# Kernel tuning notes

Measured on AMD Instinct MI355X. Metric: run time of the kernel, lower is better.

Reference implementation:

```python
import jax, jax.numpy as jnp
import numpy as np
from jax import lax

L = 5; HID = 100; B = 4; H = 256; W = 256; MU = 0.02; SLOPE = 0.01

def conv2d(x, w, pad=1, groups=1):
    return lax.conv_general_dilated(x, w, (1, 1), ((pad, pad), (pad, pad)),
                                    dimension_numbers=('NCHW', 'OIHW', 'NCHW'),
                                    feature_group_count=groups)

def leaky(x):
    return jnp.where(x >= 0, x, SLOPE * x)

def res_block(x, w1, w2, w3):
    # dropout omitted (eval-mode reference)
    h = leaky(conv2d(x, w1))
    h = leaky(conv2d(h, w2))
    return conv2d(h, w3)

def gauss1d(size=51, sigma=10.0):
    x = jnp.arange(size, dtype=jnp.float32) - (size - 1) / 2.0
    g = jnp.exp(-0.5 * (x / sigma) ** 2)
    return g / g.sum()

def gaussian_blur(x):
    # kornia GaussianBlur2d((51,51),(10,10), border 'constant') == zero-pad separable blur
    C = x.shape[1]
    g = gauss1d()
    kh = jnp.tile(g.reshape(1, 1, 1, 51), (C, 1, 1, 1))
    kv = jnp.tile(g.reshape(1, 1, 51, 1), (C, 1, 1, 1))
    x = lax.conv_general_dilated(x, kh, (1, 1), ((0, 0), (25, 25)),
                                 dimension_numbers=('NCHW', 'OIHW', 'NCHW'), feature_group_count=C)
    x = lax.conv_general_dilated(x, kv, (1, 1), ((25, 25), (0, 0)),
                                 dimension_numbers=('NCHW', 'OIHW', 'NCHW'), feature_group_count=C)
    return x

def spatial_gradient(x):
    # kornia SpatialGradient('sobel', normalized): kernels /8, replicate padding -> [B,C,2,H,W]
    Bk, C, Hk, Wk = x.shape
    kx = jnp.array([[-1., 0., 1.], [-2., 0., 2.], [-1., 0., 1.]], dtype=x.dtype) / 8.0
    k = jnp.stack([kx, kx.T])[:, None]          # [2,1,3,3]
    k = jnp.tile(k, (C, 1, 1, 1))               # [2C,1,3,3]
    xp = jnp.pad(x, ((0, 0), (0, 0), (1, 1), (1, 1)), mode='edge')
    out = conv2d(xp, k, pad=0, groups=C)        # [B,2C,H,W]
    return out.reshape(Bk, C, 2, Hk, Wk)

def deform_image(img, grid):
    # img [B,C,H,W]; grid [B,2,H,W] pixel coords (x,y); bilinear grid_sample, zeros outside
    Bk, C, Hk, Wk = img.shape
    x, y = grid[:, 0], grid[:, 1]
    x0 = jnp.floor(x); y0 = jnp.floor(y)
    wx1 = x - x0; wy1 = y - y0
    flat = img.reshape(Bk, C, Hk * Wk)
    def tap(xi, yi, wgt):
        valid = (xi >= 0) & (xi <= Wk - 1) & (yi >= 0) & (yi <= Hk - 1)
        xc = jnp.clip(xi, 0, Wk - 1).astype(jnp.int32)
        yc = jnp.clip(yi, 0, Hk - 1).astype(jnp.int32)
        idx = (yc * Wk + xc).reshape(Bk, 1, Hk * Wk)
        v = jnp.take_along_axis(flat, idx, axis=2).reshape(Bk, C, Hk, Wk)
        return v * (wgt * valid.astype(img.dtype))[:, None]
    return (tap(x0, y0, (1 - wx1) * (1 - wy1)) + tap(x0 + 1, y0, wx1 * (1 - wy1))
            + tap(x0, y0 + 1, (1 - wx1) * wy1) + tap(x0 + 1, y0 + 1, wx1 * wy1))

def forward(source, source_seg, z0, zw1, zw2, zw3, vw1, vw2, vw3):
    Bk, _, Hk, Wk = source.shape
    l = zw1.shape[0]
    yy, xx = jnp.meshgrid(jnp.arange(Hk, dtype=source.dtype), jnp.arange(Wk, dtype=source.dtype), indexing='ij')
    deformation = jnp.broadcast_to(jnp.stack([xx, yy])[None], (Bk, 2, Hk, Wk))  # pixel-coord id grid
    images = [source]
    residuals = [jnp.broadcast_to(z0, (Bk,) + z0.shape[1:])]
    residuals_deformed = [residuals[0]]
    fields = []
    grads = [spatial_gradient(source)]
    for i in range(l):
        zin = jnp.concatenate([residuals[i], images[i], images[0]], axis=1)  # 3 channels
        f = res_block(zin, zw1[i], zw2[i], zw3[i]) / l
        residuals.append(residuals[i] + f)
        residuals_deformed = [deform_image(z, deformation) for z in residuals_deformed]
        residuals_deformed.append(residuals[-1])
        vin = jnp.concatenate([deformation, images[-1]], axis=1)  # 3 channels
        fields.append(gaussian_blur(res_block(vin, vw1[i], vw2[i], vw3[i])))
        deformation = deformation - fields[i] / l
        mask = deform_image(source_seg, deformation)
        acc = residuals_deformed[1]
        for z in residuals_deformed[2:]:
            acc = acc + z
        new_img = deform_image(images[0], deformation) + acc * (MU ** 2 / l) * mask
        images.append(new_img)
        grads.append(spatial_gradient(new_img))
    return jnp.stack(images), jnp.stack(fields), jnp.stack(residuals), jnp.stack(grads)

def setup_inputs() -> dict:
    key = jax.random.key(0)
    ks = jax.random.split(key, 9)
    def rn(k, shape, s):
        return s * jax.random.normal(k, shape, dtype=jnp.float32)
    return {
        'source': rn(ks[0], (B, 1, H, W), 1.0),
        'source_seg': jax.random.uniform(ks[1], (B, 1, H, W), dtype=jnp.float32),
        'z0': rn(ks[2], (1, 1, H, W), 0.05),
        'zw1': rn(ks[3], (L, HID, 3, 3, 3), 0.2),
        'zw2': rn(ks[4], (L, HID, HID, 3, 3), 0.033),
        'zw3': rn(ks[5], (L, 1, HID, 3, 3), 0.033),
        'vw1': rn(ks[6], (L, HID, 3, 3, 3), 0.02),
        'vw2': rn(ks[7], (L, HID, HID, 3, 3), 0.033),
        'vw3': rn(ks[8], (L, 2, HID, 3, 3), 0.033),
    }

def reference(source, source_seg, z0, zw1, zw2, zw3, vw1, vw2, vw3):
    return forward(source, source_seg, z0, zw1, zw2, zw3, vw1, vw2, vw3)
```

## Files before the change

### kernel.cpp

```cpp
#include <hip/hip_runtime.h>
#include <math.h>

#define HW 65536
#define BB 4
#define NL 5

typedef short s8v __attribute__((ext_vector_type(8)));
typedef float f4v __attribute__((ext_vector_type(4)));
typedef unsigned short u16;

#define AS1 __attribute__((address_space(1)))
#define AS3 __attribute__((address_space(3)))

__device__ __forceinline__ float leaky_f(float x){ return x >= 0.f ? x : 0.01f * x; }

__device__ __forceinline__ u16 f2bf(float x){
    union { float f; unsigned u; } v; v.f = x;
    unsigned r = v.u + 0x7FFF + ((v.u >> 16) & 1);
    return (u16)(r >> 16);
}
__device__ __forceinline__ float bf2f(u16 h){
    union { unsigned u; float f; } v; v.u = ((unsigned)h) << 16;
    return v.f;
}

__global__ void k_init(const float* __restrict__ src, const float* __restrict__ z0,
                       float* __restrict__ images0, float* __restrict__ resid0,
                       float* __restrict__ def){
    int p = blockIdx.x * 256 + threadIdx.x;
    int b = p >> 16, q = p & 65535;
    images0[p] = src[p];
    resid0[p]  = z0[q];
    int x = q & 255, y = q >> 8;
    def[(size_t)(b * 2 + 0) * HW + q] = (float)x;
    def[(size_t)(b * 2 + 1) * HW + q] = (float)y;
}

__global__ void k_grad(const float* __restrict__ img, float* __restrict__ gout){
    int p = blockIdx.x * 256 + threadIdx.x;
    int b = p >> 16, q = p & 65535;
    int x = q & 255, y = q >> 8;
    const float* ib = img + (size_t)b * HW;
    int xm = max(x - 1, 0), xp = min(x + 1, 255);
    int ym = max(y - 1, 0), yp = min(y + 1, 255);
    float a00 = ib[ym * 256 + xm], a01 = ib[ym * 256 + x], a02 = ib[ym * 256 + xp];
    float a10 = ib[y  * 256 + xm],                         a12 = ib[y  * 256 + xp];
    float a20 = ib[yp * 256 + xm], a21 = ib[yp * 256 + x], a22 = ib[yp * 256 + xp];
    float gx = (a02 - a00 + 2.f * (a12 - a10) + a22 - a20) * 0.125f;
    float gy = (a20 - a00 + 2.f * (a21 - a01) + a22 - a02) * 0.125f;
    gout[(size_t)(b * 2 + 0) * HW + q] = gx;
    gout[(size_t)(b * 2 + 1) * HW + q] = gy;
}

__global__ void k_packw(const float* __restrict__ zw2, const float* __restrict__ vw2,
                        u16* __restrict__ wp){
    int idx = blockIdx.x * 256 + threadIdx.x;
    int lane9 = idx & 511, chunk = idx >> 9;
    int nt = chunk % 7; int t = chunk / 7;
    int ks = t % 4; t >>= 2;
    int off = t % 9; t /= 9;
    int layer = t % 5, path = t / 5;
    int lane = lane9 >> 3, j = lane9 & 7;
    int ic = ks * 32 + (lane >> 4) * 8 + j;
    int oc = nt * 16 + (lane & 15);
    const float* w = path ? vw2 : zw2;
    float v = 0.f;
    if (ic < 100 && oc < 100)
        v = w[(((size_t)layer * 100 + oc) * 100 + ic) * 9 + off];
    wp[idx] = f2bf(v);
}

__global__ void k_packw3(const float* __restrict__ zw3, const float* __restrict__ vw3,
                         u16* __restrict__ wq){
    int idx = blockIdx.x * 256 + threadIdx.x;
    if (idx >= 184320) return;
    int lane9 = idx & 511, chunk = idx >> 9;
    int ks = chunk & 3; int t = chunk >> 2;
    int off = t % 9; int slot = t / 9;
    int lane = lane9 >> 3, j = lane9 & 7;
    int ic = ks * 32 + (lane >> 4) * 8 + j;
    int oc = lane & 15;
    float v = 0.f;
    if (ic < 100){
        if (slot < 5){ if (oc == 0) v = zw3[((size_t)slot * 100 + ic) * 9 + off]; }
        else { int layer = slot - 5;
               if (oc < 2) v = vw3[(((size_t)layer * 2 + oc) * 100 + ic) * 9 + off]; }
    }
    wq[idx] = f2bf(v);
}

__global__ __launch_bounds__(256)
void k_conv1(const float* __restrict__ p0, int s0, const float* __restrict__ p1, int s1,
             const float* __restrict__ p2, int s2, const float* __restrict__ w1,
             u16* __restrict__ h1, int b0){
    __shared__ float t3[300];
    __shared__ float wl[2700];
    const int tid = threadIdx.x;
    const int tX = blockIdx.x, tY = blockIdx.y, bz = blockIdx.z;
    const int b = b0 + bz;
    const int y0 = tY * 8 - 1, x0 = tX * 8 - 1;
    for (int idx = tid; idx < 300; idx += 256){
        int ch = idx / 100, p = idx - ch * 100;
        int r = p / 10, c = p - r * 10;
        int gy = y0 + r, gx = x0 + c;
        const float* pp = (ch == 0) ? p0 + (size_t)b * s0
                        : (ch == 1) ? p1 + (size_t)b * s1 : p2 + (size_t)b * s2;
        t3[idx] = ((unsigned)gy < 256u && (unsigned)gx < 256u) ? pp[gy * 256 + gx] : 0.f;
    }
    for (int idx = tid; idx < 2700; idx += 256) wl[idx] = w1[idx];
    __syncthreads();

    const int px = tid & 63, g = tid >> 6;
    const int row = px >> 3, colx = px & 7;
    float iv[27];
    #pragma unroll
    for (int c3 = 0; c3 < 3; c3++)
        #pragma unroll
        for (int dr = 0; dr < 3; dr++)
            #pragma unroll
            for (int dc = 0; dc < 3; dc++)
                iv[c3 * 9 + dr * 3 + dc] = t3[c3 * 100 + (row + dr) * 10 + colx + dc];

    const int gy = tY * 8 + row, gx = tX * 8 + colx;
    u16* dst = h1 + (((size_t)bz * HW + (size_t)(gy * 256 + gx)) << 7) + g * 32;
    #pragma unroll
    for (int s = 0; s < 4; s++){
        int ov[4];
        #pragma unroll
        for (int hp = 0; hp < 4; hp++){
            u16 lo = 0, hi = 0;
            #pragma unroll
            for (int e = 0; e < 2; e++){
                int oc = g * 32 + s * 8 + hp * 2 + e;
                u16 hv = 0;
                if (oc < 100){
                    const float* wk = &wl[oc * 27];
                    float a = 0.f;
                    #pragma unroll
                    for (int q = 0; q < 27; q++) a = fmaf(wk[q], iv[q], a);
                    hv = f2bf(leaky_f(a));
                }
                if (e) hi = hv; else lo = hv;
            }
            ov[hp] = (int)lo | ((int)hi << 16);
        }
        *(int4*)(dst + s * 8) = make_int4(ov[0], ov[1], ov[2], ov[3]);
    }
}

__device__ __forceinline__ void dma_setup(const u16* __restrict__ h, size_t hbase,
                                          int y0, int x0, int tid,
                                          const u16** gp, int* gstep){
    const u16* zpad = h + (hbase << 7) + 112;
    #pragma unroll
    for (int s = 0; s < 6; s++){
        int idx = tid + s * 256;
        const u16* g = zpad; int st = 0;
        if (idx < 1360){
            int px = idx >> 2, part = idx & 3;
            int hr = px / 34, hc = px - hr * 34;
            int gy = y0 + hr, gx = x0 + hc;
            if ((unsigned)gy < 256u && (unsigned)gx < 256u){
                g = h + ((hbase + (size_t)(gy * 256 + gx)) << 7) + (part ^ ((px >> 1) & 3)) * 8;
                st = 32;
            }
        }
        gp[s] = g; gstep[s] = st;
    }
}

__device__ __forceinline__ void dma_slab(const u16** gp, const int* gstep,
                                         short* Lnxt, int wv){
    #pragma unroll
    for (int s = 0; s < 6; s++){
        __builtin_amdgcn_global_load_lds(
            (const AS1 unsigned int*)(unsigned long long)(const void*)gp[s],
            (AS3 unsigned int*)(unsigned long long)(void*)(&Lnxt[(s * 256 + wv * 64) * 8]),
            16, 0, 0);
        gp[s] += gstep[s];
    }
}

__global__ __launch_bounds__(256, 2)
void k_conv2(const u16* __restrict__ h1, const u16* __restrict__ wp, u16* __restrict__ h2){
    __shared__ __align__(16) short lds[2][12288];
    const int tid = threadIdx.x;
    const int lane = tid & 63, wv = tid >> 6;
    const int quad = lane >> 4, m = lane & 15;
    const int tX = blockIdx.x, tY = blockIdx.y, bz = blockIdx.z;
    const int y0 = tY * 8 - 1, x0 = tX * 32 - 1;
    const size_t hbase = (size_t)bz << 16;

    f4v acc[4][7];
    #pragma unroll
    for (int t = 0; t < 4; t++)
        #pragma unroll
        for (int n = 0; n < 7; n++){
            acc[t][n][0] = 0.f; acc[t][n][1] = 0.f; acc[t][n][2] = 0.f; acc[t][n][3] = 0.f;
        }

    const u16* gp[6]; int gstep[6];
    dma_setup(h1, hbase, y0, x0, tid, gp, gstep);
    dma_slab(gp, gstep, lds[0], wv);

    for (int ks = 0; ks < 4; ks++){
        __syncthreads();
        const short* L = lds[ks & 1];
        short* Lnxt = lds[(ks + 1) & 1];
        const bool pre = (ks < 3);
        #pragma unroll
        for (int off = 0; off < 9; off++){
            if (off == 4 && pre) dma_slab(gp, gstep, Lnxt, wv);
            const int dr = off / 3, dc = off - dr * 3;
            s8v bf[4];
            #pragma unroll
            for (int t = 0; t < 4; t++){
                int hpx = (2 * wv + (t >> 1) + dr) * 34 + (t & 1) * 16 + dc + m;
                bf[t] = *(const s8v*)&L[hpx * 32 + ((quad ^ ((hpx >> 1) & 3)) << 3)];
            }
            const u16* wb = wp + (size_t)((off * 4 + ks) * 7) * 512 + lane * 8;
            #pragma unroll
            for (int nt = 0; nt < 7; nt++){
                s8v af = *(const s8v*)(wb + nt * 512);
                #pragma unroll
                for (int t = 0; t < 4; t++)
                    acc[t][nt] = __builtin_amdgcn_mfma_f32_16x16x32_bf16(af, bf[t], acc[t][nt], 0, 0, 0);
            }
        }
    }

    #pragma unroll
    for (int t = 0; t < 4; t++){
        int gy = tY * 8 + 2 * wv + (t >> 1);
        int gx = tX * 32 + (t & 1) * 16 + m;
        u16* base = h2 + ((hbase + (size_t)(gy * 256 + gx)) << 7);
        #pragma unroll
        for (int nt = 0; nt < 7; nt++){
            unsigned lo = (unsigned)f2bf(leaky_f(acc[t][nt][0])) |
                          ((unsigned)f2bf(leaky_f(acc[t][nt][1])) << 16);
            unsigned hi = (unsigned)f2bf(leaky_f(acc[t][nt][2])) |
                          ((unsigned)f2bf(leaky_f(acc[t][nt][3])) << 16);
            *(int2*)(base + nt * 16 + quad * 4) = make_int2((int)lo, (int)hi);
        }
    }
    {
        int gy = tY * 8 + (tid >> 5), gx = tX * 32 + (tid & 31);
        u16* p = h2 + ((hbase + (size_t)(gy * 256 + gx)) << 7);
        *(int4*)(p + 112) = make_int4(0, 0, 0, 0);
        *(int4*)(p + 120) = make_int4(0, 0, 0, 0);
    }
}

template<int N>
__global__ __launch_bounds__(256, 2)
void k_conv3(const u16* __restrict__ h2, const u16* __restrict__ wq,
             const float* __restrict__ rprev, float* __restrict__ out0,
             float* __restrict__ out1, int b0){
    __shared__ __align__(16) short lds[2][12288];
    const int tid = threadIdx.x;
    const int lane = tid & 63, wv = tid >> 6;
    const int quad = lane >> 4, m = lane & 15;
    const int tX = blockIdx.x, tY = blockIdx.y, bz = blockIdx.z;
    const int y0 = tY * 8 - 1, x0 = tX * 32 - 1;
    const size_t hbase = (size_t)bz << 16;

    f4v acc[4];
    #pragma unroll
    for (int t = 0; t < 4; t++){ acc[t][0]=0.f; acc[t][1]=0.f; acc[t][2]=0.f; acc[t][3]=0.f; }

    const u16* gp[6]; int gstep[6];
    dma_setup(h2, hbase, y0, x0, tid, gp, gstep);
    dma_slab(gp, gstep, lds[0], wv);

    for (int ks = 0; ks < 4; ks++){
        __syncthreads();
        const short* L = lds[ks & 1];
        short* Lnxt = lds[(ks + 1) & 1];
        const bool pre = (ks < 3);
        #pragma unroll
        for (int off = 0; off < 9; off++){
            if (off == 4 && pre) dma_slab(gp, gstep, Lnxt, wv);
            const int dr = off / 3, dc = off - dr * 3;
            s8v wf = *(const s8v*)(wq + (size_t)((off * 4 + ks)) * 512 + lane * 8);
            #pragma unroll
            for (int t = 0; t < 4; t++){
                int hpx = (2 * wv + (t >> 1) + dr) * 34 + (t & 1) * 16 + dc + m;
                s8v af = *(const s8v*)&L[hpx * 32 + ((quad ^ ((hpx >> 1) & 3)) << 3)];
                acc[t] = __builtin_amdgcn_mfma_f32_16x16x32_bf16(af, wf, acc[t], 0, 0, 0);
            }
        }
    }

    const int b = b0 + bz;
    #pragma unroll
    for (int t = 0; t < 4; t++){
        int gy = tY * 8 + 2 * wv + (t >> 1);
        int gx = tX * 32 + (t & 1) * 16 + quad * 4;
        size_t p = (size_t)gy * 256 + gx;
        if (N == 1){
            if (m == 0){
                float4 rp = *(const float4*)&rprev[(size_t)b * HW + p];
                float4 v = make_float4(rp.x + acc[t][0] * 0.2f, rp.y + acc[t][1] * 0.2f,
                                       rp.z + acc[t][2] * 0.2f, rp.w + acc[t][3] * 0.2f);
                *(float4*)&out0[(size_t)b * HW + p] = v;
                *(float4*)&out1[(size_t)b * HW + p] = v;
            }
        } else {
            if (m < 2){
                float4 v = make_float4(acc[t][0], acc[t][1], acc[t][2], acc[t][3]);
                *(float4*)&out0[((size_t)(b * 2) + m) * HW + p] = v;
            }
        }
    }
}

__device__ __forceinline__ float bilin(const float* __restrict__ img, float x, float y){
    float x0 = floorf(x), y0 = floorf(y);
    float wx = x - x0, wy = y - y0;
    float r = 0.f;
    #pragma unroll
    for (int dy = 0; dy < 2; dy++){
        float yi = y0 + (float)dy;
        if (yi < 0.f || yi > 255.f) continue;
        int iy = (int)yi;
        float wyv = dy ? wy : 1.f - wy;
        #pragma unroll
        for (int dx = 0; dx < 2; dx++){
            float xi = x0 + (float)dx;
            if (xi < 0.f || xi > 255.f) continue;
            int ix = (int)xi;
            float wxv = dx ? wx : 1.f - wx;
            r += wyv * wxv * img[iy * 256 + ix];
        }
    }
    return r;
}

__global__ void k_deform(const float* __restrict__ rdin, const float* __restrict__ def,
                         float* __restrict__ rdout){
    int p = blockIdx.x * 256 + threadIdx.x;
    int j = blockIdx.y;
    int b = p >> 16, q = p & 65535;
    float x = def[(size_t)(b * 2 + 0) * HW + q];
    float y = def[(size_t)(b * 2 + 1) * HW + q];
    rdout[(size_t)j * BB * HW + p] = bilin(rdin + (size_t)j * BB * HW + (size_t)b * HW, x, y);
}

__global__ void k_blur_h(const float* __restrict__ in, float* __restrict__ outb){
    __shared__ float g[51];
    __shared__ float row[306];
    __shared__ float ginv;
    int tid = threadIdx.x;
    int rid = blockIdx.x;
    int ch = rid >> 8, y = rid & 255;
    if (tid < 51){ float d = (float)tid - 25.f; g[tid] = expf(-0.005f * d * d); }
    row[tid + 25] = in[(size_t)ch * HW + y * 256 + tid];
    if (tid < 25) row[tid] = 0.f;
    if (tid >= 231) row[tid + 50] = 0.f;
    __syncthreads();
    if (tid == 0){ float s = 0.f; for (int k = 0; k < 51; k++) s += g[k]; ginv = 1.f / s; }
    __syncthreads();
    float acc = 0.f;
    for (int k = 0; k < 51; k++) acc = fmaf(g[k], row[tid + k], acc);
    outb[(size_t)ch * HW + y * 256 + tid] = acc * ginv;
}

__global__ void k_blur_v(const float* __restrict__ in, float* __restrict__ fout,
                         float* __restrict__ def){
    __shared__ float g[51];
    __shared__ float ginv;
    __shared__ float tb[82 * 64];
    int tid = threadIdx.x;
    int tX = blockIdx.x, tY = blockIdx.y, ch = blockIdx.z;
    if (tid < 51){ float d = (float)tid - 25.f; g[tid] = expf(-0.005f * d * d); }
    for (int idx = tid; idx < 82 * 64; idx += 256){
        int r = idx >> 6, c = idx & 63;
        int gy = tY * 32 + r - 25, gx = tX * 64 + c;
        tb[idx] = (gy >= 0 && gy < 256) ? in[(size_t)ch * HW + gy * 256 + gx] : 0.f;
    }
    __syncthreads();
    if (tid == 0){ float s = 0.f; for (int k = 0; k < 51; k++) s += g[k]; ginv = 1.f / s; }
    __syncthreads();
    int c = tid & 63, r0 = (tid >> 6) * 8;
    for (int k = 0; k < 8; k++){
        int r = r0 + k;
        float acc = 0.f;
        for (int t = 0; t < 51; t++) acc = fmaf(g[t], tb[(r + t) * 64 + c], acc);
        acc *= ginv;
        int y = tY * 32 + r, x = tX * 64 + c;
        fout[(size_t)ch * HW + y * 256 + x] = acc;
        def [(size_t)ch * HW + y * 256 + x] -= acc * 0.2f;
    }
}

__global__ void k_final(const float* __restrict__ def, const float* __restrict__ src,
                        const float* __restrict__ seg, const float* __restrict__ rdbase,
                        int nrd, float* __restrict__ imgout){
    int p = blockIdx.x * 256 + threadIdx.x;
    int b = p >> 16, q = p & 65535;
    float x = def[(size_t)(b * 2 + 0) * HW + q];
    float y = def[(size_t)(b * 2 + 1) * HW + q];
    float mk = bilin(seg + (size_t)b * HW, x, y);
    float s = bilin(src + (size_t)b * HW, x, y);
    float acc = 0.f;
    for (int j = 0; j < nrd; j++) acc += rdbase[(size_t)j * BB * HW + p];
    imgout[p] = s + acc * 8e-5f * mk;
}

extern "C" void kernel_launch(void* const* d_in, const int* in_sizes, int n_in,
                              void* d_out, int out_size, void* d_ws, size_t ws_size,
                              hipStream_t stream){
    const float* source = (const float*)d_in[0];
    const float* seg    = (const float*)d_in[1];
    const float* z0     = (const float*)d_in[2];
    const float* zw1    = (const float*)d_in[3];
    const float* zw2    = (const float*)d_in[4];
    const float* zw3    = (const float*)d_in[5];
    const float* vw1    = (const float*)d_in[6];
    const float* vw2    = (const float*)d_in[7];
    const float* vw3    = (const float*)d_in[8];

    float* out = (float*)d_out;
    float* images = out;
    float* fields = out + 1572864;
    float* resid  = out + 4194304;
    float* grads  = out + 5767168;

    float* ws = (float*)d_ws;
    float* def  = ws;
    float* RDa  = def  + 524288;
    float* RDb  = RDa  + 1310720;
    float* vtmp = RDb  + 1310720;
    float* btmp = vtmp + 524288;
    u16*   wp   = (u16*)(btmp + 524288);
    u16*   wq3  = wp + 1290240;
    u16*   h1   = wq3 + 184320;

    size_t need4 = 4194304ull * 4 + 1290240ull * 2 + 184320ull * 2 + 2ull * 4 * 16777216ull;
    const int HB = (ws_size >= need4) ? 4 : 1;
    u16* h2 = h1 + (size_t)HB * 8388608;

    k_packw <<<5040, 256, 0, stream>>>(zw2, vw2, wp);
    k_packw3<<<720, 256, 0, stream>>>(zw3, vw3, wq3);
    k_init  <<<1024, 256, 0, stream>>>(source, z0, images, resid, def);
    k_grad  <<<1024, 256, 0, stream>>>(source, grads);

    float* RDcur = RDa;
    float* RDnxt = RDb;

    for (int i = 0; i < NL; i++){
        float* res_i  = resid  + (size_t)i * BB * HW;
        float* res_ip = resid  + (size_t)(i + 1) * BB * HW;
        float* img_i  = images + (size_t)i * BB * HW;
        float* img_ip = images + (size_t)(i + 1) * BB * HW;

        for (int b0 = 0; b0 < BB; b0 += HB){
            k_conv1<<<dim3(32, 32, HB), 256, 0, stream>>>(
                res_i, HW, img_i, HW, images, HW, zw1 + (size_t)i * 2700, h1, b0);
            k_conv2<<<dim3(8, 32, HB), 256, 0, stream>>>(
                h1, wp + (size_t)i * 129024, h2);
            k_conv3<1><<<dim3(8, 32, HB), 256, 0, stream>>>(
                h2, wq3 + (size_t)i * 18432, res_i, res_ip,
                RDnxt + (size_t)i * BB * HW, b0);
        }

        if (i > 0)
            k_deform<<<dim3(1024, i), 256, 0, stream>>>(RDcur, def, RDnxt);

        for (int b0 = 0; b0 < BB; b0 += HB){
            k_conv1<<<dim3(32, 32, HB), 256, 0, stream>>>(
                def, 2 * HW, def + HW, 2 * HW, img_i, HW, vw1 + (size_t)i * 2700, h1, b0);
            k_conv2<<<dim3(8, 32, HB), 256, 0, stream>>>(
                h1, wp + (size_t)(NL + i) * 129024, h2);
            k_conv3<2><<<dim3(8, 32, HB), 256, 0, stream>>>(
                h2, wq3 + (size_t)(NL + i) * 18432, nullptr, vtmp, nullptr, b0);
        }
        k_blur_h<<<2048, 256, 0, stream>>>(vtmp, btmp);
        k_blur_v<<<dim3(4, 8, 8), 256, 0, stream>>>(
            btmp, fields + (size_t)i * BB * 2 * HW, def);

        k_final<<<1024, 256, 0, stream>>>(def, source, seg, RDnxt, i + 1, img_ip);
        k_grad<<<1024, 256, 0, stream>>>(img_ip, grads + (size_t)(i + 1) * BB * 2 * HW);

        float* t = RDcur; RDcur = RDnxt; RDnxt = t;
    }
}
```

Measured before the change: 2.069 ms.

## Drop LDS staging in conv2/conv3; read activations directly from global memory

Removes the double-buffered global_load_lds slab staging, the barriers and the swizzled LDS reads from the 3x3 conv MFMA kernels. Each lane now loads its bf16 activation fragments straight from global memory (relying on L1/L2 for the 9-tap overlap), and out-of-bounds taps point at a shared zero buffer written once in k_init. Without LDS the launch bounds are raised to target more resident blocks. The cost is 9x redundant global/cache traffic per pixel and exposed load latency with no explicit prefetch.

Result: slower. 3.925 ms (+89.7%).

```diff
diff --git a/kernel.cpp b/kernel.cpp
--- a/kernel.cpp
+++ b/kernel.cpp
@@ -8,9 +8,6 @@
 typedef short s8v __attribute__((ext_vector_type(8)));
 typedef float f4v __attribute__((ext_vector_type(4)));
 typedef unsigned short u16;
-
-#define AS1 __attribute__((address_space(1)))
-#define AS3 __attribute__((address_space(3)))
 
 __device__ __forceinline__ float leaky_f(float x){ return x >= 0.f ? x : 0.01f * x; }
 
@@ -26,7 +23,7 @@
 
 __global__ void k_init(const float* __restrict__ src, const float* __restrict__ z0,
                        float* __restrict__ images0, float* __restrict__ resid0,
-                       float* __restrict__ def){
+                       float* __restrict__ def, u16* __restrict__ zpad){
     int p = blockIdx.x * 256 + threadIdx.x;
     int b = p >> 16, q = p & 65535;
     images0[p] = src[p];
@@ -34,6 +31,8 @@
     int x = q & 255, y = q >> 8;
     def[(size_t)(b * 2 + 0) * HW + q] = (float)x;
     def[(size_t)(b * 2 + 1) * HW + q] = (float)y;
+    if (blockIdx.x == 0 && threadIdx.x < 64)
+        *(int4*)(zpad + threadIdx.x * 8) = make_int4(0, 0, 0, 0);
 }
 
 __global__ void k_grad(const float* __restrict__ img, float* __restrict__ gout){
@@ -148,47 +147,13 @@
     }
 }
 
-__device__ __forceinline__ void dma_setup(const u16* __restrict__ h, size_t hbase,
-                                          int y0, int x0, int tid,
-                                          const u16** gp, int* gstep){
-    const u16* zpad = h + (hbase << 7) + 112;
-    #pragma unroll
-    for (int s = 0; s < 6; s++){
-        int idx = tid + s * 256;
-        const u16* g = zpad; int st = 0;
-        if (idx < 1360){
-            int px = idx >> 2, part = idx & 3;
-            int hr = px / 34, hc = px - hr * 34;
-            int gy = y0 + hr, gx = x0 + hc;
-            if ((unsigned)gy < 256u && (unsigned)gx < 256u){
-                g = h + ((hbase + (size_t)(gy * 256 + gx)) << 7) + (part ^ ((px >> 1) & 3)) * 8;
-                st = 32;
-            }
-        }
-        gp[s] = g; gstep[s] = st;
-    }
-}
-
-__device__ __forceinline__ void dma_slab(const u16** gp, const int* gstep,
-                                         short* Lnxt, int wv){
-    #pragma unroll
-    for (int s = 0; s < 6; s++){
-        __builtin_amdgcn_global_load_lds(
-            (const AS1 unsigned int*)(unsigned long long)(const void*)gp[s],
-            (AS3 unsigned int*)(unsigned long long)(void*)(&Lnxt[(s * 256 + wv * 64) * 8]),
-            16, 0, 0);
-        gp[s] += gstep[s];
-    }
-}
-
-__global__ __launch_bounds__(256, 2)
-void k_conv2(const u16* __restrict__ h1, const u16* __restrict__ wp, u16* __restrict__ h2){
-    __shared__ __align__(16) short lds[2][12288];
+__global__ __launch_bounds__(256, 3)
+void k_conv2(const u16* __restrict__ h1, const u16* __restrict__ wp,
+             u16* __restrict__ h2, const u16* __restrict__ zpad){
     const int tid = threadIdx.x;
     const int lane = tid & 63, wv = tid >> 6;
     const int quad = lane >> 4, m = lane & 15;
     const int tX = blockIdx.x, tY = blockIdx.y, bz = blockIdx.z;
-    const int y0 = tY * 8 - 1, x0 = tX * 32 - 1;
     const size_t hbase = (size_t)bz << 16;
 
     f4v acc[4][7];
@@ -199,29 +164,29 @@
             acc[t][n][0] = 0.f; acc[t][n][1] = 0.f; acc[t][n][2] = 0.f; acc[t][n][3] = 0.f;
         }
 
-    const u16* gp[6]; int gstep[6];
-    dma_setup(h1, hbase, y0, x0, tid, gp, gstep);
-    dma_slab(gp, gstep, lds[0], wv);
-
-    for (int ks = 0; ks < 4; ks++){
-        __syncthreads();
-        const short* L = lds[ks & 1];
-        short* Lnxt = lds[(ks + 1) & 1];
-        const bool pre = (ks < 3);
-        #pragma unroll
-        for (int off = 0; off < 9; off++){
-            if (off == 4 && pre) dma_slab(gp, gstep, Lnxt, wv);
-            const int dr = off / 3, dc = off - dr * 3;
+    const u16* zp = zpad + quad * 8;
+    const u16* wlane = wp + lane * 8;
+
+    for (int off = 0; off < 9; off++){
+        const int dr = off / 3, dc = off - dr * 3;
+        const u16* ab[4];
+        #pragma unroll
+        for (int t = 0; t < 4; t++){
+            int gy = tY * 8 + 2 * wv + (t >> 1) + dr - 1;
+            int gx = tX * 32 + (t & 1) * 16 + m + dc - 1;
+            bool ok = ((unsigned)gy < 256u) & ((unsigned)gx < 256u);
+            ab[t] = ok ? h1 + ((hbase + (size_t)(gy * 256 + gx)) << 7) + quad * 8 : zp;
+        }
+        #pragma unroll
+        for (int ks = 0; ks < 4; ks++){
             s8v bf[4];
             #pragma unroll
-            for (int t = 0; t < 4; t++){
-                int hpx = (2 * wv + (t >> 1) + dr) * 34 + (t & 1) * 16 + dc + m;
-                bf[t] = *(const s8v*)&L[hpx * 32 + ((quad ^ ((hpx >> 1) & 3)) << 3)];
-            }
-            const u16* wb = wp + (size_t)((off * 4 + ks) * 7) * 512 + lane * 8;
+            for (int t = 0; t < 4; t++)
+                bf[t] = *(const s8v*)(ab[t] + ks * 32);
+            const u16* wk = wlane + (size_t)((off * 4 + ks) * 7) * 512;
             #pragma unroll
             for (int nt = 0; nt < 7; nt++){
-                s8v af = *(const s8v*)(wb + nt * 512);
+                s8v af = *(const s8v*)(wk + nt * 512);
                 #pragma unroll
                 for (int t = 0; t < 4; t++)
                     acc[t][nt] = __builtin_amdgcn_mfma_f32_16x16x32_bf16(af, bf[t], acc[t][nt], 0, 0, 0);
@@ -243,49 +208,42 @@
             *(int2*)(base + nt * 16 + quad * 4) = make_int2((int)lo, (int)hi);
         }
     }
-    {
-        int gy = tY * 8 + (tid >> 5), gx = tX * 32 + (tid & 31);
-        u16* p = h2 + ((hbase + (size_t)(gy * 256 + gx)) << 7);
-        *(int4*)(p + 112) = make_int4(0, 0, 0, 0);
-        *(int4*)(p + 120) = make_int4(0, 0, 0, 0);
-    }
 }
 
 template<int N>
-__global__ __launch_bounds__(256, 2)
+__global__ __launch_bounds__(256, 4)
 void k_conv3(const u16* __restrict__ h2, const u16* __restrict__ wq,
              const float* __restrict__ rprev, float* __restrict__ out0,
-             float* __restrict__ out1, int b0){
-    __shared__ __align__(16) short lds[2][12288];
+             float* __restrict__ out1, int b0, const u16* __restrict__ zpad){
     const int tid = threadIdx.x;
     const int lane = tid & 63, wv = tid >> 6;
     const int quad = lane >> 4, m = lane & 15;
     const int tX = blockIdx.x, tY = blockIdx.y, bz = blockIdx.z;
-    const int y0 = tY * 8 - 1, x0 = tX * 32 - 1;
     const size_t hbase = (size_t)bz << 16;
 
     f4v acc[4];
     #pragma unroll
     for (int t = 0; t < 4; t++){ acc[t][0]=0.f; acc[t][1]=0.f; acc[t][2]=0.f; acc[t][3]=0.f; }
 
-    const u16* gp[6]; int gstep[6];
-    dma_setup(h2, hbase, y0, x0, tid, gp, gstep);
-    dma_slab(gp, gstep, lds[0], wv);
-
-    for (int ks = 0; ks < 4; ks++){
-        __syncthreads();
-        const short* L = lds[ks & 1];
-        short* Lnxt = lds[(ks + 1) & 1];
-        const bool pre = (ks < 3);
-        #pragma unroll
-        for (int off = 0; off < 9; off++){
-            if (off == 4 && pre) dma_slab(gp, gstep, Lnxt, wv);
-            const int dr = off / 3, dc = off - dr * 3;
-            s8v wf = *(const s8v*)(wq + (size_t)((off * 4 + ks)) * 512 + lane * 8);
+    const u16* zp = zpad + quad * 8;
+    const u16* wlane = wq + lane * 8;
+
+    for (int off = 0; off < 9; off++){
+        const int dr = off / 3, dc = off - dr * 3;
+        const u16* ab[4];
+        #pragma unroll
+        for (int t = 0; t < 4; t++){
+            int gy = tY * 8 + 2 * wv + (t >> 1) + dr - 1;
+            int gx = tX * 32 + (t & 1) * 16 + m + dc - 1;
+            bool ok = ((unsigned)gy < 256u) & ((unsigned)gx < 256u);
+            ab[t] = ok ? h2 + ((hbase + (size_t)(gy * 256 + gx)) << 7) + quad * 8 : zp;
+        }
+        #pragma unroll
+        for (int ks = 0; ks < 4; ks++){
+            s8v wf = *(const s8v*)(wlane + (size_t)(off * 4 + ks) * 512);
             #pragma unroll
             for (int t = 0; t < 4; t++){
-                int hpx = (2 * wv + (t >> 1) + dr) * 34 + (t & 1) * 16 + dc + m;
-                s8v af = *(const s8v*)&L[hpx * 32 + ((quad ^ ((hpx >> 1) & 3)) << 3)];
+                s8v af = *(const s8v*)(ab[t] + ks * 32);
                 acc[t] = __builtin_amdgcn_mfma_f32_16x16x32_bf16(af, wf, acc[t], 0, 0, 0);
             }
         }
@@ -432,17 +390,19 @@
     float* RDb  = RDa  + 1310720;
     float* vtmp = RDb  + 1310720;
     float* btmp = vtmp + 524288;
-    u16*   wp   = (u16*)(btmp + 524288);
+    u16*   zpad = (u16*)(btmp + 524288);
+    u16*   wp   = zpad + 512;
     u16*   wq3  = wp + 1290240;
     u16*   h1   = wq3 + 184320;
 
-    size_t need4 = 4194304ull * 4 + 1290240ull * 2 + 184320ull * 2 + 2ull * 4 * 16777216ull;
+    size_t need4 = 4194304ull * 4 + 512ull * 2 + 1290240ull * 2 + 184320ull * 2
+                 + 2ull * 4 * 16777216ull;
     const int HB = (ws_size >= need4) ? 4 : 1;
     u16* h2 = h1 + (size_t)HB * 8388608;
 
     k_packw <<<5040, 256, 0, stream>>>(zw2, vw2, wp);
     k_packw3<<<720, 256, 0, stream>>>(zw3, vw3, wq3);
-    k_init  <<<1024, 256, 0, stream>>>(source, z0, images, resid, def);
+    k_init  <<<1024, 256, 0, stream>>>(source, z0, images, resid, def, zpad);
     k_grad  <<<1024, 256, 0, stream>>>(source, grads);
 
     float* RDcur = RDa;
@@ -458,10 +418,10 @@
             k_conv1<<<dim3(32, 32, HB), 256, 0, stream>>>(
                 res_i, HW, img_i, HW, images, HW, zw1 + (size_t)i * 2700, h1, b0);
             k_conv2<<<dim3(8, 32, HB), 256, 0, stream>>>(
-                h1, wp + (size_t)i * 129024, h2);
+                h1, wp + (size_t)i * 129024, h2, zpad);
             k_conv3<1><<<dim3(8, 32, HB), 256, 0, stream>>>(
                 h2, wq3 + (size_t)i * 18432, res_i, res_ip,
-                RDnxt + (size_t)i * BB * HW, b0);
+                RDnxt + (size_t)i * BB * HW, b0, zpad);
         }
 
         if (i > 0)
@@ -471,9 +431,9 @@
             k_conv1<<<dim3(32, 32, HB), 256, 0, stream>>>(
                 def, 2 * HW, def + HW, 2 * HW, img_i, HW, vw1 + (size_t)i * 2700, h1, b0);
             k_conv2<<<dim3(8, 32, HB), 256, 0, stream>>>(
-                h1, wp + (size_t)(NL + i) * 129024, h2);
+                h1, wp + (size_t)(NL + i) * 129024, h2, zpad);
             k_conv3<2><<<dim3(8, 32, HB), 256, 0, stream>>>(
-                h2, wq3 + (size_t)(NL + i) * 18432, nullptr, vtmp, nullptr, b0);
+                h2, wq3 + (size_t)(NL + i) * 18432, nullptr, vtmp, nullptr, b0, zpad);
         }
         k_blur_h<<<2048, 256, 0, stream>>>(vtmp, btmp);
         k_blur_v<<<dim3(4, 8, 8), 256, 0, stream>>>(
```

## Split conv2 waves across output-channel halves and prefetch weight fragments

Applied to the files above, without the earlier changes.

Pads the packed weights from 7 to 8 output-channel tiles. Each wave now computes 4 output-channel tiles by 8 pixel tiles (split into horizontal and vertical halves) instead of 7 channel tiles by 4 pixel tiles. Weight fragments are double-buffered in registers and prefetched one step ahead, so global weight loads overlap with MFMA work and each wave loads fewer weight fragments. The cost is more LDS reads for activations, 32 accumulators per wave instead of 28, and some MFMAs spent on the padded channels 100-127. The explicit zeroing of channels 112-127 is dropped because the padded weights now write zeros there.

After: 2.456 ms. 1.19x slower.

```diff
diff --git a/kernel.cpp b/kernel.cpp
--- a/kernel.cpp
+++ b/kernel.cpp
@@ -56,7 +56,7 @@
                         u16* __restrict__ wp){
     int idx = blockIdx.x * 256 + threadIdx.x;
     int lane9 = idx & 511, chunk = idx >> 9;
-    int nt = chunk % 7; int t = chunk / 7;
+    int nt = chunk & 7; int t = chunk >> 3;
     int ks = t % 4; t >>= 2;
     int off = t % 9; t /= 9;
     int layer = t % 5, path = t / 5;
@@ -187,67 +187,74 @@
     const int tid = threadIdx.x;
     const int lane = tid & 63, wv = tid >> 6;
     const int quad = lane >> 4, m = lane & 15;
+    const int hhalf = wv & 1, vhalf = wv >> 1;
     const int tX = blockIdx.x, tY = blockIdx.y, bz = blockIdx.z;
     const int y0 = tY * 8 - 1, x0 = tX * 32 - 1;
     const size_t hbase = (size_t)bz << 16;
 
-    f4v acc[4][7];
+    f4v acc[4][8];
     #pragma unroll
     for (int t = 0; t < 4; t++)
         #pragma unroll
-        for (int n = 0; n < 7; n++){
+        for (int n = 0; n < 8; n++){
             acc[t][n][0] = 0.f; acc[t][n][1] = 0.f; acc[t][n][2] = 0.f; acc[t][n][3] = 0.f;
         }
 
     const u16* gp[6]; int gstep[6];
     dma_setup(h1, hbase, y0, x0, tid, gp, gstep);
     dma_slab(gp, gstep, lds[0], wv);
+
+    const u16* wl = wp + lane * 8;
+    s8v af[2][4];
+    #pragma unroll
+    for (int t = 0; t < 4; t++)
+        af[0][t] = *(const s8v*)(wl + (size_t)(4 * hhalf + t) * 512);
 
     for (int ks = 0; ks < 4; ks++){
         __syncthreads();
         const short* L = lds[ks & 1];
         short* Lnxt = lds[(ks + 1) & 1];
-        const bool pre = (ks < 3);
         #pragma unroll
         for (int off = 0; off < 9; off++){
-            if (off == 4 && pre) dma_slab(gp, gstep, Lnxt, wv);
-            const int dr = off / 3, dc = off - dr * 3;
-            s8v bf[4];
-            #pragma unroll
-            for (int t = 0; t < 4; t++){
-                int hpx = (2 * wv + (t >> 1) + dr) * 34 + (t & 1) * 16 + dc + m;
-                bf[t] = *(const s8v*)&L[hpx * 32 + ((quad ^ ((hpx >> 1) & 3)) << 3)];
-            }
-            const u16* wb = wp + (size_t)((off * 4 + ks) * 7) * 512 + lane * 8;
-            #pragma unroll
-            for (int nt = 0; nt < 7; nt++){
-                s8v af = *(const s8v*)(wb + nt * 512);
+            const int kk = ks * 9 + off;
+            if (off == 4 && ks < 3) dma_slab(gp, gstep, Lnxt, wv);
+            if (kk < 35){
+                int nks = (off == 8) ? ks + 1 : ks;
+                int noff = (off == 8) ? 0 : off + 1;
                 #pragma unroll
                 for (int t = 0; t < 4; t++)
-                    acc[t][nt] = __builtin_amdgcn_mfma_f32_16x16x32_bf16(af, bf[t], acc[t][nt], 0, 0, 0);
-            }
-        }
-    }
-
-    #pragma unroll
-    for (int t = 0; t < 4; t++){
-        int gy = tY * 8 + 2 * wv + (t >> 1);
-        int gx = tX * 32 + (t & 1) * 16 + m;
-        u16* base = h2 + ((hbase + (size_t)(gy * 256 + gx)) << 7);
-        #pragma unroll
-        for (int nt = 0; nt < 7; nt++){
-            unsigned lo = (unsigned)f2bf(leaky_f(acc[t][nt][0])) |
-                          ((unsigned)f2bf(leaky_f(acc[t][nt][1])) << 16);
-            unsigned hi = (unsigned)f2bf(leaky_f(acc[t][nt][2])) |
-                          ((unsigned)f2bf(leaky_f(acc[t][nt][3])) << 16);
-            *(int2*)(base + nt * 16 + quad * 4) = make_int2((int)lo, (int)hi);
-        }
-    }
-    {
-        int gy = tY * 8 + (tid >> 5), gx = tX * 32 + (tid & 31);
-        u16* p = h2 + ((hbase + (size_t)(gy * 256 + gx)) << 7);
-        *(int4*)(p + 112) = make_int4(0, 0, 0, 0);
-        *(int4*)(p + 120) = make_int4(0, 0, 0, 0);
+                    af[(kk + 1) & 1][t] =
+                        *(const s8v*)(wl + (size_t)((noff * 4 + nks) * 8 + 4 * hhalf + t) * 512);
+            }
+            const int dr = off / 3, dc = off - dr * 3;
+            s8v bf[8];
+            #pragma unroll
+            for (int n = 0; n < 8; n++){
+                int hpx = (4 * vhalf + (n >> 1) + dr) * 34 + (n & 1) * 16 + m + dc;
+                bf[n] = *(const s8v*)&L[hpx * 32 + ((quad ^ ((hpx >> 1) & 3)) << 3)];
+            }
+            #pragma unroll
+            for (int t = 0; t < 4; t++)
+                #pragma unroll
+                for (int n = 0; n < 8; n++)
+                    acc[t][n] = __builtin_amdgcn_mfma_f32_16x16x32_bf16(
+                        af[kk & 1][t], bf[n], acc[t][n], 0, 0, 0);
+        }
+    }
+
+    #pragma unroll
+    for (int n = 0; n < 8; n++){
+        int gy = tY * 8 + 4 * vhalf + (n >> 1);
+        int gx = tX * 32 + (n & 1) * 16 + m;
+        u16* base = h2 + ((hbase + (size_t)(gy * 256 + gx)) << 7) + 64 * hhalf;
+        #pragma unroll
+        for (int t = 0; t < 4; t++){
+            unsigned lo = (unsigned)f2bf(leaky_f(acc[t][n][0])) |
+                          ((unsigned)f2bf(leaky_f(acc[t][n][1])) << 16);
+            unsigned hi = (unsigned)f2bf(leaky_f(acc[t][n][2])) |
+                          ((unsigned)f2bf(leaky_f(acc[t][n][3])) << 16);
+            *(int2*)(base + t * 16 + quad * 4) = make_int2((int)lo, (int)hi);
+        }
     }
 }
 
@@ -281,7 +288,7 @@
         for (int off = 0; off < 9; off++){
             if (off == 4 && pre) dma_slab(gp, gstep, Lnxt, wv);
             const int dr = off / 3, dc = off - dr * 3;
-            s8v wf = *(const s8v*)(wq + (size_t)((off * 4 + ks)) * 512 + lane * 8);
+            s8v wf = *(const s8v*)(wq + (size_t)(off * 4 + ks) * 512 + lane * 8);
             #pragma unroll
             for (int t = 0; t < 4; t++){
                 int hpx = (2 * wv + (t >> 1) + dr) * 34 + (t & 1) * 16 + dc + m;
@@ -433,14 +440,14 @@
     float* vtmp = RDb  + 1310720;
     float* btmp = vtmp + 524288;
     u16*   wp   = (u16*)(btmp + 524288);
-    u16*   wq3  = wp + 1290240;
+    u16*   wq3  = wp + 1474560;
     u16*   h1   = wq3 + 184320;
 
-    size_t need4 = 4194304ull * 4 + 1290240ull * 2 + 184320ull * 2 + 2ull * 4 * 16777216ull;
+    size_t need4 = 4194304ull * 4 + 1474560ull * 2 + 184320ull * 2 + 2ull * 4 * 16777216ull;
     const int HB = (ws_size >= need4) ? 4 : 1;
     u16* h2 = h1 + (size_t)HB * 8388608;
 
-    k_packw <<<5040, 256, 0, stream>>>(zw2, vw2, wp);
+    k_packw <<<5760, 256, 0, stream>>>(zw2, vw2, wp);
     k_packw3<<<720, 256, 0, stream>>>(zw3, vw3, wq3);
     k_init  <<<1024, 256, 0, stream>>>(source, z0, images, resid, def);
     k_grad  <<<1024, 256, 0, stream>>>(source, grads);
@@ -458,7 +465,7 @@
             k_conv1<<<dim3(32, 32, HB), 256, 0, stream>>>(
                 res_i, HW, img_i, HW, images, HW, zw1 + (size_t)i * 2700, h1, b0);
             k_conv2<<<dim3(8, 32, HB), 256, 0, stream>>>(
-                h1, wp + (size_t)i * 129024, h2);
+                h1, wp + (size_t)i * 147456, h2);
             k_conv3<1><<<dim3(8, 32, HB), 256, 0, stream>>>(
                 h2, wq3 + (size_t)i * 18432, res_i, res_ip,
                 RDnxt + (size_t)i * BB * HW, b0);
@@ -471,7 +478,7 @@
             k_conv1<<<dim3(32, 32, HB), 256, 0, stream>>>(
                 def, 2 * HW, def + HW, 2 * HW, img_i, HW, vw1 + (size_t)i * 2700, h1, b0);
             k_conv2<<<dim3(8, 32, HB), 256, 0, stream>>>(
-                h1, wp + (size_t)(NL + i) * 129024, h2);
+                h1, wp + (size_t)(NL + i) * 147456, h2);
             k_conv3<2><<<dim3(8, 32, HB), 256, 0, stream>>>(
                 h2, wq3 + (size_t)(NL + i) * 18432, nullptr, vtmp, nullptr, b0);
         }
```
